# Performance work log

Measured on AMD Instinct MI355X. Metric: run time of the kernel, lower is better.

Reference implementation:

```python
import jax, jax.numpy as jnp
import numpy as np
from jax import lax

K = 3          # kernel_size
STRIDE = 2
BN_EPS = 1e-5
CLAMP_MIN = 1e-4


def setup_inputs() -> dict:
    key = jax.random.key(0)
    k1, k2 = jax.random.split(key)
    x = jax.random.normal(k1, (16, 64, 112, 112), dtype=jnp.float32)
    # kaiming-normal fan_out init: std = sqrt(2 / (out_ch * kh * kw))
    std = np.sqrt(2.0 / (9 * 3 * 3)).astype(np.float32)
    conv_w = jax.random.normal(k2, (9, 64, 3, 3), dtype=jnp.float32) * std
    gamma = jnp.ones((9,), dtype=jnp.float32)
    beta = jnp.zeros((9,), dtype=jnp.float32)
    return {"x": x, "conv_w": conv_w, "gamma": gamma, "beta": beta}


def reference(x, conv_w, gamma, beta):
    p = K // 2
    n, c, h, w = x.shape
    xp = jnp.pad(x, ((0, 0), (0, 0), (p, p), (p, p)), mode="reflect")  # [n,c,h+2p,w+2p]

    # sigma = BN(conv(pad(x))) with 3x3 conv, stride 1, no bias -> [n, k*k, h, w]
    sigma = lax.conv_general_dilated(
        xp, conv_w, window_strides=(1, 1), padding="VALID",
        dimension_numbers=("NCHW", "OIHW", "NCHW"))
    mean = jnp.mean(sigma, axis=(0, 2, 3), keepdims=True)
    var = jnp.var(sigma, axis=(0, 2, 3), keepdims=True)
    sigma = (sigma - mean) * lax.rsqrt(var + BN_EPS)
    sigma = sigma * gamma[None, :, None, None] + beta[None, :, None, None]
    sigma = jnp.clip(sigma, CLAMP_MIN)               # clamp(min=1e-4)
    sigma = sigma / jnp.sum(sigma, axis=1, keepdims=True)  # normalize over k*k taps

    # unfold pad(x) into k*k patches -> [n, c*k*k, h, w] (channel-major like torch unfold)
    patches = lax.conv_general_dilated_patches(
        xp, filter_shape=(K, K), window_strides=(1, 1), padding="VALID",
        dimension_numbers=("NCHW", "OIHW", "NCHW"))
    patches = patches.reshape(n, c, K * K, h, w)

    out = jnp.sum(patches * sigma[:, None], axis=2)  # [n, c, h, w]
    return out[:, :, ::STRIDE, ::STRIDE]
```

## Files before the change

### kernel.cpp

```cpp
#include <hip/hip_runtime.h>
#include <math.h>

namespace {

constexpr int Hh = 112, Ww = 112, Cc = 64, Nn = 16;
constexpr int OHh = 56, OWw = 56;
constexpr int HW = Hh * Ww;
constexpr int OP = OHh * OWw;
constexpr int NP = Nn * OP;
constexpr int NHW = Nn * HW;
constexpr float BN_EPS_F = 1e-5f;
constexpr float CLAMP_MIN_F = 1e-4f;
constexpr int NSTAT = 32;

template <int NSPLIT>
__global__ __launch_bounds__(256) void conv_split_kernel(
    const float* __restrict__ x, const float* __restrict__ wgt,
    float* __restrict__ P )
{
    constexpr int CHS = Cc / NSPLIT;
    constexpr int NBLK = NSPLIT * 392;

    const int tid = threadIdx.x;
    const int b = blockIdx.x;
    const int swz = (b & 7) * (NBLK / 8) + (b >> 3);
    const int part = swz / 392;
    const int bid = swz - part * 392;

    const int s = bid * 256 + tid;
    const int pos0 = 2 * s;
    const int n = pos0 / HW;
    const int hw = pos0 - n * HW;
    const int h = hw / Ww;
    const int w0 = hw - h * Ww;

    const int hm = (h == 0) ? 1 : h - 1;
    const int hp = (h == Hh - 1) ? (Hh - 2) : (h + 1);
    const int wl = (w0 == 0) ? 1 : w0 - 1;
    const int wr = (w0 == Ww - 2) ? (Ww - 2) : (w0 + 2);

    const int ro[3] = { hm * Ww, h * Ww, hp * Ww };

    const float* xb = x + ((size_t)n * Cc + part * CHS) * HW;

    float m0[3], m1[3], el[3], er[3];
    float n_m0[3], n_m1[3], n_el[3], n_er[3];
#pragma unroll
    for (int r = 0; r < 3; ++r) {
        const float2 f2 = *(const float2*)(xb + ro[r] + w0);
        m0[r] = f2.x; m1[r] = f2.y;
        el[r] = xb[ro[r] + wl];
        er[r] = xb[ro[r] + wr];
    }

    float acc0[9], acc1[9];
#pragma unroll
    for (int k = 0; k < 9; ++k) { acc0[k] = 0.f; acc1[k] = 0.f; }

#pragma unroll 2
    for (int c = 0; c < CHS; ++c) {
        const float* xn = xb + (size_t)((c + 1) & (CHS - 1)) * HW;
#pragma unroll
        for (int r = 0; r < 3; ++r) {
            const float2 f2 = *(const float2*)(xn + ro[r] + w0);
            n_m0[r] = f2.x; n_m1[r] = f2.y;
            n_el[r] = xn[ro[r] + wl];
            n_er[r] = xn[ro[r] + wr];
        }

        const int cg = part * CHS + c;
#pragma unroll
        for (int k = 0; k < 9; ++k) {
            const float* wk = wgt + ((size_t)k * Cc + cg) * 9;
#pragma unroll
            for (int r = 0; r < 3; ++r) {
                const float wa = wk[3 * r], wb = wk[3 * r + 1], wc = wk[3 * r + 2];
                acc0[k] = fmaf(wa, el[r], acc0[k]);
                acc0[k] = fmaf(wb, m0[r], acc0[k]);
                acc0[k] = fmaf(wc, m1[r], acc0[k]);
                acc1[k] = fmaf(wa, m0[r], acc1[k]);
                acc1[k] = fmaf(wb, m1[r], acc1[k]);
                acc1[k] = fmaf(wc, er[r], acc1[k]);
            }
        }

#pragma unroll
        for (int r = 0; r < 3; ++r) {
            m0[r] = n_m0[r]; m1[r] = n_m1[r];
            el[r] = n_el[r]; er[r] = n_er[r];
        }
    }

    float* Ph = P + (size_t)part * 9 * NHW;
#pragma unroll
    for (int k = 0; k < 9; ++k)
        *(float2*)(Ph + (size_t)k * NHW + pos0) = make_float2(acc0[k], acc1[k]);
}

template <int NSPLIT>
__global__ __launch_bounds__(256) void merge_stats_kernel(
    const float* __restrict__ P, double* __restrict__ stats,
    float* __restrict__ sig_even )
{
    __shared__ float rs[4], rq[4];
    const int tid = threadIdx.x;
    const int k = blockIdx.y;
    const int p0 = (blockIdx.x * 256 + tid) * 4;

    float4 v = *(const float4*)(P + (size_t)k * NHW + p0);
#pragma unroll
    for (int qq = 1; qq < NSPLIT; ++qq) {
        const float4 t = *(const float4*)(P + ((size_t)qq * 9 + k) * NHW + p0);
        v.x += t.x; v.y += t.y; v.z += t.z; v.w += t.w;
    }

    const int w = p0 % Ww;
    const int h = (p0 / Ww) % Hh;
    const int n = p0 / HW;
    if (!(h & 1)) {
        *(float2*)(sig_even + (size_t)k * NP + n * OP + (h >> 1) * OWw + (w >> 1)) =
            make_float2(v.x, v.z);
    }

    float s = v.x + v.y + v.z + v.w;
    float q = v.x * v.x + v.y * v.y + v.z * v.z + v.w * v.w;
#pragma unroll
    for (int off = 32; off > 0; off >>= 1) {
        s += __shfl_down(s, off, 64);
        q += __shfl_down(q, off, 64);
    }
    const int lane = tid & 63, wv = tid >> 6;
    if (lane == 0) { rs[wv] = s; rq[wv] = q; }
    __syncthreads();
    if (tid == 0) {
        double* st = stats + (size_t)(blockIdx.x & (NSTAT - 1)) * 18;
        atomicAdd(&st[k], (double)(rs[0] + rs[1] + rs[2] + rs[3]));
        atomicAdd(&st[9 + k], (double)(rq[0] + rq[1] + rq[2] + rq[3]));
    }
}

__global__ __launch_bounds__(256) void apply_kernel(
    const float* __restrict__ x, const float* __restrict__ sig_raw,
    const float* __restrict__ gamma, const float* __restrict__ beta,
    const double* __restrict__ stats, float* __restrict__ out)
{
    __shared__ float srow[9][OWw];
    __shared__ float mean_s[9], istd_s[9], gb[18];

    const int tid = threadIdx.x;
    const int f = blockIdx.x;
    const int fs = (f & 7) * 112 + (f >> 3);
    const int n = fs / OHh;
    const int oh = fs % OHh;

    if (tid < 9) {
        double s = 0.0, q = 0.0;
        for (int r = 0; r < NSTAT; ++r) { s += stats[r * 18 + tid]; q += stats[r * 18 + 9 + tid]; }
        const double cnt = (double)Nn * HW;
        const double m = s / cnt;
        const double v = q / cnt - m * m;
        mean_s[tid] = (float)m;
        istd_s[tid] = (float)(1.0 / sqrt(v + (double)BN_EPS_F));
        gb[tid] = gamma[tid];
        gb[9 + tid] = beta[tid];
    }
    __syncthreads();

    if (tid < OWw) {
        const int pp = n * OP + oh * OWw + tid;
        float s[9], ssum = 0.f;
#pragma unroll
        for (int k = 0; k < 9; ++k) {
            float v = fmaf((sig_raw[(size_t)k * NP + pp] - mean_s[k]) * istd_s[k], gb[k], gb[9 + k]);
            v = fmaxf(v, CLAMP_MIN_F);
            s[k] = v;
            ssum += v;
        }
        const float inv = 1.f / ssum;
#pragma unroll
        for (int k = 0; k < 9; ++k) srow[k][tid] = s[k] * inv;
    }
    __syncthreads();

    const int csub = tid >> 6;
    const int lane = tid & 63;
    if (lane >= OWw) return;
    const int ow = lane;

    const int r0 = (oh == 0) ? 1 : (2 * oh - 1);
    const int r1 = 2 * oh, r2 = 2 * oh + 1;
    const int c0 = (ow == 0) ? 1 : (2 * ow - 1);
    const int c1 = 2 * ow, c2 = 2 * ow + 1;

    float sg[9];
#pragma unroll
    for (int k = 0; k < 9; ++k) sg[k] = srow[k][ow];

#pragma unroll 2
    for (int cc = 0; cc < 16; ++cc) {
        const int c = cc * 4 + csub;
        const float* xc = x + ((size_t)(n * Cc + c)) * HW;
        float o = 0.f;
        o = fmaf(sg[0], xc[r0 * Ww + c0], o);
        o = fmaf(sg[1], xc[r0 * Ww + c1], o);
        o = fmaf(sg[2], xc[r0 * Ww + c2], o);
        o = fmaf(sg[3], xc[r1 * Ww + c0], o);
        o = fmaf(sg[4], xc[r1 * Ww + c1], o);
        o = fmaf(sg[5], xc[r1 * Ww + c2], o);
        o = fmaf(sg[6], xc[r2 * Ww + c0], o);
        o = fmaf(sg[7], xc[r2 * Ww + c1], o);
        o = fmaf(sg[8], xc[r2 * Ww + c2], o);
        out[((size_t)(n * Cc + c)) * OP + oh * OWw + ow] = o;
    }
}

}

extern "C" void kernel_launch(void* const* d_in, const int* in_sizes, int n_in,
                              void* d_out, int out_size, void* d_ws, size_t ws_size,
                              hipStream_t stream) {
    const float* x     = (const float*)d_in[0];
    const float* wgt   = (const float*)d_in[1];
    const float* gamma = (const float*)d_in[2];
    const float* beta  = (const float*)d_in[3];
    float* out = (float*)d_out;

    double* stats = (double*)d_ws;
    float* P = (float*)((char*)d_ws + 8192);

    const size_t sig_bytes = (size_t)9 * NP * 4;
    const size_t need4 = 8192 + (size_t)36 * NHW * 4 + sig_bytes;
    hipMemsetAsync(d_ws, 0, 8192, stream);

    if (ws_size >= need4) {
        float* sig_even = P + (size_t)36 * NHW;
        conv_split_kernel<4><<<1568, 256, 0, stream>>>(x, wgt, P);
        merge_stats_kernel<4><<<dim3(196, 9), 256, 0, stream>>>(P, stats, sig_even);
        apply_kernel<<<896, 256, 0, stream>>>(x, sig_even, gamma, beta, stats, out);
    } else {
        float* sig_even = P + (size_t)18 * NHW;
        conv_split_kernel<2><<<784, 256, 0, stream>>>(x, wgt, P);
        merge_stats_kernel<2><<<dim3(196, 9), 256, 0, stream>>>(P, stats, sig_even);
        apply_kernel<<<896, 256, 0, stream>>>(x, sig_even, gamma, beta, stats, out);
    }
}
```

Measured before the change: 71.42 us.

## Stream conv input rows through an LDS ring with async global-to-LDS loads

Rewrites the conv kernel so each wavefront handles one output row. It stages three input rows per channel into a per-wave LDS ring using global_load_lds, keeps 6 channels in flight, and waits on vmcnt before computing each channel. The channel split is fixed at 2 and the workspace-dependent 4-way path is removed, so merge_stats now sums only two partials. The aim is to hide global load latency and coalesce row loads. The cost is fewer blocks, idle lanes (56 of 64 active), and fully unrolled code that raises register pressure.

```diff
diff --git a/kernel.cpp b/kernel.cpp
--- a/kernel.cpp
+++ b/kernel.cpp
@@ -12,92 +12,127 @@
 constexpr float BN_EPS_F = 1e-5f;
 constexpr float CLAMP_MIN_F = 1e-4f;
 constexpr int NSTAT = 32;
-
-template <int NSPLIT>
-__global__ __launch_bounds__(256) void conv_split_kernel(
+constexpr int CHS = 32;
+constexpr int DEPTH = 6;
+constexpr int RING = 8;
+
+__device__ __forceinline__ void gload_lds16(const float* g, float* l) {
+    __builtin_amdgcn_global_load_lds(
+        (const __attribute__((address_space(1))) void*)g,
+        (__attribute__((address_space(3))) void*)l, 16, 0, 0);
+}
+
+__device__ __forceinline__ void compute_from_lds(
+    const float* __restrict__ buf, const float* __restrict__ wgt, int cg,
+    int w0, int wm1, int wp2, float (&acc0)[9], float (&acc1)[9])
+{
+    float lft[3], rgt[3];
+    float2 mid[3];
+#pragma unroll
+    for (int r = 0; r < 3; ++r) {
+        mid[r] = *(const float2*)(buf + r * Ww + w0);
+        lft[r] = buf[r * Ww + wm1];
+        rgt[r] = buf[r * Ww + wp2];
+    }
+#pragma unroll
+    for (int k = 0; k < 9; ++k) {
+        const float* wk = wgt + ((size_t)k * Cc + cg) * 9;
+#pragma unroll
+        for (int r = 0; r < 3; ++r) {
+            const float wa = wk[3 * r], wb = wk[3 * r + 1], wc = wk[3 * r + 2];
+            acc0[k] = fmaf(wa, lft[r],   acc0[k]);
+            acc0[k] = fmaf(wb, mid[r].x, acc0[k]);
+            acc0[k] = fmaf(wc, mid[r].y, acc0[k]);
+            acc1[k] = fmaf(wa, mid[r].x, acc1[k]);
+            acc1[k] = fmaf(wb, mid[r].y, acc1[k]);
+            acc1[k] = fmaf(wc, rgt[r],   acc1[k]);
+        }
+    }
+}
+
+__global__ __launch_bounds__(256) void conv_lds_kernel(
     const float* __restrict__ x, const float* __restrict__ wgt,
     float* __restrict__ P )
 {
-    constexpr int CHS = Cc / NSPLIT;
-    constexpr int NBLK = NSPLIT * 392;
+    __shared__ __align__(16) float ring[4][RING][3 * Ww];
 
     const int tid = threadIdx.x;
+    const int lane = tid & 63;
+    const int wv = tid >> 6;
+
     const int b = blockIdx.x;
-    const int swz = (b & 7) * (NBLK / 8) + (b >> 3);
-    const int part = swz / 392;
-    const int bid = swz - part * 392;
-
-    const int s = bid * 256 + tid;
-    const int pos0 = 2 * s;
-    const int n = pos0 / HW;
-    const int hw = pos0 - n * HW;
-    const int h = hw / Ww;
-    const int w0 = hw - h * Ww;
-
-    const int hm = (h == 0) ? 1 : h - 1;
-    const int hp = (h == Hh - 1) ? (Hh - 2) : (h + 1);
-    const int wl = (w0 == 0) ? 1 : w0 - 1;
-    const int wr = (w0 == Ww - 2) ? (Ww - 2) : (w0 + 2);
-
-    const int ro[3] = { hm * Ww, h * Ww, hp * Ww };
+    const int swz = (b & 7) * 112 + (b >> 3);
+    const int part = swz / 448;
+    const int rem = swz - part * 448;
+    const int n = rem / 28;
+    const int h = (rem % 28) * 4 + wv;
+
+    const int rs0 = (h == 0) ? 1 : h - 1;
+    const int rs2 = (h == Hh - 1) ? (Hh - 2) : h + 1;
+
+    int so0, so1 = 0;
+    {
+        const int r = lane / 28, k = lane - r * 28;
+        const int row = (r == 0) ? rs0 : ((r == 1) ? h : rs2);
+        so0 = row * Ww + k * 4;
+    }
+    const bool act1 = (lane < 20);
+    if (act1) {
+        const int s1 = lane + 64;
+        const int r = s1 / 28, k = s1 - r * 28;
+        const int row = (r == 1) ? h : rs2;
+        so1 = ((s1 / 28 == 2) ? rs2 : ((s1 / 28 == 1) ? h : rs0)) * Ww + k * 4;
+        (void)row;
+    }
 
     const float* xb = x + ((size_t)n * Cc + part * CHS) * HW;
 
-    float m0[3], m1[3], el[3], er[3];
-    float n_m0[3], n_m1[3], n_el[3], n_er[3];
-#pragma unroll
-    for (int r = 0; r < 3; ++r) {
-        const float2 f2 = *(const float2*)(xb + ro[r] + w0);
-        m0[r] = f2.x; m1[r] = f2.y;
-        el[r] = xb[ro[r] + wl];
-        er[r] = xb[ro[r] + wr];
-    }
+    const int l = (lane < 56) ? lane : 55;
+    const int w0 = 2 * l;
+    const int wm1 = (w0 == 0) ? 1 : w0 - 1;
+    const int wp2 = (w0 + 1 == Ww - 1) ? (Ww - 2) : (w0 + 2);
 
     float acc0[9], acc1[9];
 #pragma unroll
     for (int k = 0; k < 9; ++k) { acc0[k] = 0.f; acc1[k] = 0.f; }
 
-#pragma unroll 2
-    for (int c = 0; c < CHS; ++c) {
-        const float* xn = xb + (size_t)((c + 1) & (CHS - 1)) * HW;
-#pragma unroll
-        for (int r = 0; r < 3; ++r) {
-            const float2 f2 = *(const float2*)(xn + ro[r] + w0);
-            n_m0[r] = f2.x; n_m1[r] = f2.y;
-            n_el[r] = xn[ro[r] + wl];
-            n_er[r] = xn[ro[r] + wr];
-        }
-
-        const int cg = part * CHS + c;
-#pragma unroll
-        for (int k = 0; k < 9; ++k) {
-            const float* wk = wgt + ((size_t)k * Cc + cg) * 9;
-#pragma unroll
-            for (int r = 0; r < 3; ++r) {
-                const float wa = wk[3 * r], wb = wk[3 * r + 1], wc = wk[3 * r + 2];
-                acc0[k] = fmaf(wa, el[r], acc0[k]);
-                acc0[k] = fmaf(wb, m0[r], acc0[k]);
-                acc0[k] = fmaf(wc, m1[r], acc0[k]);
-                acc1[k] = fmaf(wa, m0[r], acc1[k]);
-                acc1[k] = fmaf(wb, m1[r], acc1[k]);
-                acc1[k] = fmaf(wc, er[r], acc1[k]);
-            }
-        }
-
-#pragma unroll
-        for (int r = 0; r < 3; ++r) {
-            m0[r] = n_m0[r]; m1[r] = n_m1[r];
-            el[r] = n_el[r]; er[r] = n_er[r];
-        }
-    }
-
-    float* Ph = P + (size_t)part * 9 * NHW;
-#pragma unroll
-    for (int k = 0; k < 9; ++k)
-        *(float2*)(Ph + (size_t)k * NHW + pos0) = make_float2(acc0[k], acc1[k]);
-}
-
-template <int NSPLIT>
+#define STAGE(c)                                                                \
+    {                                                                           \
+        const float* src = xb + (size_t)(c) * HW;                               \
+        float* dst = &ring[wv][(c) & (RING - 1)][0];                            \
+        gload_lds16(src + so0, dst);                                            \
+        if (act1) gload_lds16(src + so1, dst + 256);                            \
+    }
+
+    STAGE(0) STAGE(1) STAGE(2) STAGE(3) STAGE(4) STAGE(5)
+
+#define WAITN(c) (((c) + DEPTH < CHS) ? (2 * DEPTH) : (2 * (CHS - 1 - (c))))
+#define STEP(c)                                                                 \
+    {                                                                           \
+        if constexpr ((c) + DEPTH < CHS) STAGE((c) + DEPTH)                     \
+        asm volatile("s_waitcnt vmcnt(%0)" ::"i"(WAITN(c)) : "memory");         \
+        __builtin_amdgcn_sched_barrier(0);                                      \
+        compute_from_lds(&ring[wv][(c) & (RING - 1)][0], wgt,                   \
+                         part * CHS + (c), w0, wm1, wp2, acc0, acc1);           \
+    }
+
+    STEP(0)  STEP(1)  STEP(2)  STEP(3)  STEP(4)  STEP(5)  STEP(6)  STEP(7)
+    STEP(8)  STEP(9)  STEP(10) STEP(11) STEP(12) STEP(13) STEP(14) STEP(15)
+    STEP(16) STEP(17) STEP(18) STEP(19) STEP(20) STEP(21) STEP(22) STEP(23)
+    STEP(24) STEP(25) STEP(26) STEP(27) STEP(28) STEP(29) STEP(30) STEP(31)
+#undef STEP
+#undef WAITN
+#undef STAGE
+
+    if (lane < 56) {
+        const int pos0 = n * HW + h * Ww + w0;
+        float* Ph = P + (size_t)part * 9 * NHW;
+#pragma unroll
+        for (int k = 0; k < 9; ++k)
+            *(float2*)(Ph + (size_t)k * NHW + pos0) = make_float2(acc0[k], acc1[k]);
+    }
+}
+
 __global__ __launch_bounds__(256) void merge_stats_kernel(
     const float* __restrict__ P, double* __restrict__ stats,
     float* __restrict__ sig_even )
@@ -108,9 +143,8 @@
     const int p0 = (blockIdx.x * 256 + tid) * 4;
 
     float4 v = *(const float4*)(P + (size_t)k * NHW + p0);
-#pragma unroll
-    for (int qq = 1; qq < NSPLIT; ++qq) {
-        const float4 t = *(const float4*)(P + ((size_t)qq * 9 + k) * NHW + p0);
+    {
+        const float4 t = *(const float4*)(P + ((size_t)9 + k) * NHW + p0);
         v.x += t.x; v.y += t.y; v.z += t.z; v.w += t.w;
     }
 
@@ -129,8 +163,8 @@
         s += __shfl_down(s, off, 64);
         q += __shfl_down(q, off, 64);
     }
-    const int lane = tid & 63, wv = tid >> 6;
-    if (lane == 0) { rs[wv] = s; rq[wv] = q; }
+    const int lane = tid & 63, wvv = tid >> 6;
+    if (lane == 0) { rs[wvv] = s; rq[wvv] = q; }
     __syncthreads();
     if (tid == 0) {
         double* st = stats + (size_t)(blockIdx.x & (NSTAT - 1)) * 18;
@@ -227,20 +261,10 @@
 
     double* stats = (double*)d_ws;
     float* P = (float*)((char*)d_ws + 8192);
-
-    const size_t sig_bytes = (size_t)9 * NP * 4;
-    const size_t need4 = 8192 + (size_t)36 * NHW * 4 + sig_bytes;
+    float* sig_even = P + (size_t)18 * NHW;
+
     hipMemsetAsync(d_ws, 0, 8192, stream);
-
-    if (ws_size >= need4) {
-        float* sig_even = P + (size_t)36 * NHW;
-        conv_split_kernel<4><<<1568, 256, 0, stream>>>(x, wgt, P);
-        merge_stats_kernel<4><<<dim3(196, 9), 256, 0, stream>>>(P, stats, sig_even);
-        apply_kernel<<<896, 256, 0, stream>>>(x, sig_even, gamma, beta, stats, out);
-    } else {
-        float* sig_even = P + (size_t)18 * NHW;
-        conv_split_kernel<2><<<784, 256, 0, stream>>>(x, wgt, P);
-        merge_stats_kernel<2><<<dim3(196, 9), 256, 0, stream>>>(P, stats, sig_even);
-        apply_kernel<<<896, 256, 0, stream>>>(x, sig_even, gamma, beta, stats, out);
-    }
-}
+    conv_lds_kernel<<<896, 256, 0, stream>>>(x, wgt, P);
+    merge_stats_kernel<<<dim3(196, 9), 256, 0, stream>>>(P, stats, sig_even);
+    apply_kernel<<<896, 256, 0, stream>>>(x, sig_even, gamma, beta, stats, out);
+}
```

After: 189.9 us. 2.66x slower.
